# Kernel optimization log

Hardware: AMD Instinct MI355X
Metric: run time of the kernel (lower is better)

The kernel has to match this reference:

```python
import jax, jax.numpy as jnp
import numpy as np

H, QP, VP, D, DP = 4, 4, 4, 128, 64
DH = D // H


def setup_inputs() -> dict:
    key = jax.random.key(0)
    ks = jax.random.split(key, 16)
    B, L = 1, 1024
    w_c0 = float(np.log(np.e - 1.0))
    inp = {
        'single': jax.random.normal(ks[0], (B, L, D), jnp.float32),
        'pair': jax.random.normal(ks[1], (B, L, L, DP), jnp.float32),
        'T': jax.random.normal(ks[2], (B, L, 4, 4), jnp.float32),
        'w_C': jnp.full((H,), w_c0, jnp.float32),
        'ln_g': jnp.ones((D,), jnp.float32),
        'ln_b': jnp.zeros((D,), jnp.float32),
        'Wq': jax.random.normal(ks[3], (D, H * DH), jnp.float32) * 0.05,
        'Wk': jax.random.normal(ks[4], (D, H * DH), jnp.float32) * 0.05,
        'Wv': jax.random.normal(ks[5], (D, H * DH), jnp.float32) * 0.05,
        'Wqpt': jax.random.normal(ks[6], (D, H * QP * 3), jnp.float32) * 0.05,
        'Wkpt': jax.random.normal(ks[7], (D, H * QP * 3), jnp.float32) * 0.05,
        'Wvpt': jax.random.normal(ks[8], (D, H * VP * 3), jnp.float32) * 0.05,
        'Wb': jax.random.normal(ks[9], (DP, H), jnp.float32) * 0.05,
        'Wout': jax.random.normal(ks[10], (H * (DH + DP + VP * 3 + VP), D), jnp.float32) * 0.05,
        'b_out': jnp.zeros((D,), jnp.float32),
    }
    return inp


def _layernorm(x, g, b, eps=1e-5):
    x32 = x.astype(jnp.float32)
    mu = x32.mean(-1, keepdims=True)
    var = ((x32 - mu) ** 2).mean(-1, keepdims=True)
    return ((x32 - mu) * jax.lax.rsqrt(var + eps) * g + b).astype(x.dtype)


def reference(single, pair, T, w_C, ln_g, ln_b, Wq, Wk, Wv, Wqpt, Wkpt, Wvpt, Wb, Wout, b_out):
    B, L, Dm = single.shape
    scale_attn = DH ** (-0.5)
    z = _layernorm(single, ln_g, ln_b)
    Q = (z @ Wq).reshape(B, L, H, DH)
    K = (z @ Wk).reshape(B, L, H, DH)
    V = (z @ Wv).reshape(B, L, H, DH)
    Q_pt = (z @ Wqpt).reshape(B, L, H, QP, 3)
    K_pt = (z @ Wkpt).reshape(B, L, H, QP, 3)
    V_pt = (z @ Wvpt).reshape(B, L, H, VP, 3)
    R = T[..., :3, :3]   # [B,L,3,3]
    t = T[..., :3, 3]    # [B,L,3]
    # global-frame points: R @ p + t
    Q_g = jnp.einsum('blxy,blhpy->blhpx', R, Q_pt) + t[:, :, None, None, :]
    K_g = jnp.einsum('blxy,blhpy->blhpx', R, K_pt) + t[:, :, None, None, :]
    V_g = jnp.einsum('blxy,blhpy->blhpx', R, V_pt) + t[:, :, None, None, :]
    # scalar QK score [B,H,L,L]
    s_attn = jnp.einsum('bihd,bjhd->bhij', Q, K) * scale_attn
    # pair bias [B,H,L,L]
    b_attn = jnp.einsum('bijc,ch->bhij', pair, Wb)
    # squared point distance [B,H,L,L]
    diff = Q_g[:, :, None] - K_g[:, None]          # [B,L,L,H,QP,3]
    d2 = jnp.moveaxis((diff ** 2).sum((-1, -2)), -1, 1)
    w_pt = jax.nn.softplus(w_C)[None, :, None, None]
    attn = jax.nn.softmax(s_attn + b_attn - 0.5 * w_pt * d2, axis=-1)
    # scalar values [B,L,H*DH]
    o_s = jnp.einsum('bhij,bjhd->bihd', attn, V).reshape(B, L, H * DH)
    # point values aggregated in global frame then mapped back: R^T (p - t)
    o_pt_g = jnp.einsum('bhij,bjhpx->bihpx', attn, V_g)
    o_pt = jnp.einsum('blyx,blhpy->blhpx', R, o_pt_g - t[:, :, None, None, :])
    o_pt_n = jnp.sqrt((o_pt ** 2).sum(-1))
    # pair aggregation [B,L,H*DP]
    o_pair = jnp.einsum('bhij,bijc->bihc', attn, pair).reshape(B, L, H * DP)
    out = jnp.concatenate([o_s, o_pair, o_pt.reshape(B, L, -1), o_pt_n.reshape(B, L, -1)], axis=-1)
    return single + out @ Wout + b_out
```

## Files before the change

kernel.cpp:

```cpp
#include <hip/hip_runtime.h>
#include <math.h>

#define L_SEQ 1024
#define DM 128

#define OFF_KHAT 0
#define OFF_QHAT (L_SEQ * 192)
#define OFF_V    (OFF_QHAT + L_SEQ * 192)
#define OFF_VG   (OFF_V + L_SEQ * DM)

typedef __attribute__((address_space(1))) const void* gas_t;
typedef __attribute__((address_space(3))) void* las_t;

__device__ __forceinline__ void async16(const float4* g, float4* l) {
    __builtin_amdgcn_global_load_lds((gas_t)g, (las_t)l, 16, 0, 0);
}

__global__ __launch_bounds__(256) void ipa_prep(
    const float* __restrict__ single, const float* __restrict__ T,
    const float* __restrict__ w_C, const float* __restrict__ ln_g, const float* __restrict__ ln_b,
    const float* __restrict__ Wq, const float* __restrict__ Wk, const float* __restrict__ Wv,
    const float* __restrict__ Wqpt, const float* __restrict__ Wkpt, const float* __restrict__ Wvpt,
    float* __restrict__ ws)
{
    __shared__ float z_lds[128];
    __shared__ float proj[528];
    __shared__ float qg[4][4][3];
    __shared__ float kg[4][4][3];
    __shared__ float cq[4], ck[4];

    const int t = threadIdx.x;
    const int i = blockIdx.x;

    if (t < 64) {
        float x0 = single[i*DM + t];
        float x1 = single[i*DM + 64 + t];
        float s = x0 + x1, s2 = x0*x0 + x1*x1;
        #pragma unroll
        for (int off = 1; off < 64; off <<= 1) { s += __shfl_xor(s, off); s2 += __shfl_xor(s2, off); }
        float mu = s * 0.0078125f;
        float var = s2 * 0.0078125f - mu*mu;
        float rs = rsqrtf(var + 1e-5f);
        z_lds[t]      = (x0 - mu) * rs * ln_g[t]      + ln_b[t];
        z_lds[t + 64] = (x1 - mu) * rs * ln_g[t + 64] + ln_b[t + 64];
    }
    __syncthreads();

    for (int cc = t; cc < 528; cc += 256) {
        const float* W; int col, ncol;
        if (cc < 128)      { W = Wq;   col = cc;       ncol = 128; }
        else if (cc < 256) { W = Wk;   col = cc - 128; ncol = 128; }
        else if (cc < 384) { W = Wv;   col = cc - 256; ncol = 128; }
        else if (cc < 432) { W = Wqpt; col = cc - 384; ncol = 48;  }
        else if (cc < 480) { W = Wkpt; col = cc - 432; ncol = 48;  }
        else               { W = Wvpt; col = cc - 480; ncol = 48;  }
        float a = 0.f;
        #pragma unroll 8
        for (int k = 0; k < 128; ++k)
            a = fmaf(z_lds[k], W[k*ncol + col], a);
        proj[cc] = a;
    }
    __syncthreads();

    if (t < 16) {
        int h = t >> 2, p = t & 3;
        float R[3][3], tt[3];
        #pragma unroll
        for (int x = 0; x < 3; ++x) {
            #pragma unroll
            for (int y = 0; y < 3; ++y) R[x][y] = T[i*16 + x*4 + y];
            tt[x] = T[i*16 + x*4 + 3];
        }
        int base = 384 + (h*4 + p)*3;
        float q0 = proj[base],    q1 = proj[base+1],  q2 = proj[base+2];
        float k0 = proj[base+48], k1 = proj[base+49], k2 = proj[base+50];
        float v0 = proj[base+96], v1 = proj[base+97], v2 = proj[base+98];
        #pragma unroll
        for (int x = 0; x < 3; ++x) {
            float qq = R[x][0]*q0 + R[x][1]*q1 + R[x][2]*q2 + tt[x];
            float kk = R[x][0]*k0 + R[x][1]*k1 + R[x][2]*k2 + tt[x];
            float vv = R[x][0]*v0 + R[x][1]*v1 + R[x][2]*v2 + tt[x];
            qg[h][p][x] = qq;
            kg[h][p][x] = kk;
            ws[OFF_VG + (size_t)i*48 + h*12 + p*3 + x] = vv;
        }
    }
    __syncthreads();

    if (t < 8) {
        int h = t >> 1, isk = t & 1;
        float w = w_C[h];
        float wp = log1pf(__expf(w));
        float sq = 0.f;
        #pragma unroll
        for (int p = 0; p < 4; ++p)
            #pragma unroll
            for (int x = 0; x < 3; ++x) {
                float g = isk ? kg[h][p][x] : qg[h][p][x];
                sq += g*g;
            }
        float c = -0.5f * wp * sq;
        if (isk) ck[h] = c; else cq[h] = c;
    }
    __syncthreads();

    if (t < 128) ws[OFF_V + (size_t)i*DM + t] = proj[256 + t];
    const float scale_attn = 0.17677669529663687f;
    if (t < 192) {
        int h = t / 48, k = t % 48;
        float w = w_C[h];
        float wp = log1pf(__expf(w));
        float kv, qv;
        if (k < 32) {
            kv = proj[128 + h*32 + k];
            qv = scale_attn * proj[h*32 + k];
        } else if (k < 44) {
            int e = k - 32;
            kv = kg[h][e/3][e%3];
            qv = wp * qg[h][e/3][e%3];
        } else if (k == 44) { kv = ck[h]; qv = 1.0f; }
        else if (k == 45)   { kv = 1.0f; qv = cq[h]; }
        else                { kv = 0.f;  qv = 0.f; }
        ws[OFF_KHAT + (size_t)i*192 + t] = kv;
        ws[OFF_QHAT + (size_t)i*192 + t] = qv;
    }
}

__global__ __launch_bounds__(256, 2) void ipa_attn(
    const float* __restrict__ single, const float* __restrict__ pair,
    const float* __restrict__ T, const float* __restrict__ Wb,
    const float* __restrict__ Wout, const float* __restrict__ b_out,
    const float* __restrict__ ws, float* __restrict__ out)
{
    __shared__ __align__(16) float4 pair_w[4][2][2][16][16];
    __shared__ __align__(16) float4 qhat_lds[2][4][13];
    __shared__ __align__(16) float wbt_lds[4][68];
    __shared__ __align__(16) float p_ws[4][2][16][4];

    const int t = threadIdx.x;
    const int wv = t >> 6, lane = t & 63;
    const int i0 = blockIdx.x * 2;

    if (t < 96) {
        int r = t / 48, rest = t % 48;
        qhat_lds[r][rest/12][rest%12] = ((const float4*)(ws + OFF_QHAT))[(size_t)(i0+r)*48 + rest];
    } else if (t < 160) {
        int c = t - 96;
        float4 w4 = ((const float4*)Wb)[c];
        wbt_lds[0][c] = w4.x; wbt_lds[1][c] = w4.y; wbt_lds[2][c] = w4.z; wbt_lds[3][c] = w4.w;
    }

    const int m_h  = lane & 3,  m_j  = lane >> 2;
    const int os_h = lane >> 4, os_jh = (lane >> 3) & 1, os_d4 = lane & 7;
    const int op_c4 = lane & 15, op_jq = lane >> 4;
    const int og_he = lane & 15, og_jq = lane >> 4;
    const bool og_act = og_he < 12;
    const int og_h  = (og_act ? og_he : 0) / 3;
    const int og_ix = og_act ? og_he : 0;

    float m0_run = -INFINITY, l0_run = 0.f;
    float m1_run = -INFINITY, l1_run = 0.f;
    float4 accp[2][4];
    float4 accs[2], accg[2];
    #pragma unroll
    for (int r = 0; r < 2; ++r) {
        accs[r] = make_float4(0.f,0.f,0.f,0.f);
        accg[r] = make_float4(0.f,0.f,0.f,0.f);
        #pragma unroll
        for (int h = 0; h < 4; ++h) accp[r][h] = make_float4(0.f,0.f,0.f,0.f);
    }

    const float4* pair4 = (const float4*)pair;
    const float4* kh4   = (const float4*)(ws + OFF_KHAT);
    const float4* v4    = (const float4*)(ws + OFF_V);
    const float4* vg4   = (const float4*)(ws + OFF_VG);
    float4* mypair = &pair_w[wv][0][0][0][0];

    #pragma unroll
    for (int it = 0; it < 8; ++it) {
        int idx = it*64 + lane;
        int row = idx >> 8, j = (idx >> 4) & 15, slot = idx & 15;
        int c4 = slot ^ (j & 7);
        async16(pair4 + ((size_t)(i0+row)*L_SEQ + wv*256 + j)*16 + c4, mypair + idx);
    }
    __syncthreads();

    for (int s = 0; s < 16; ++s) {
        const int cur = s & 1;
        const int j0 = wv*256 + s*16;

        float4 kh[12];
        {
            const float4* kp = kh4 + (size_t)(j0 + m_j)*48 + m_h*12;
            #pragma unroll
            for (int k4 = 0; k4 < 12; ++k4) kh[k4] = kp[k4];
        }
        float4 vv[8];
        #pragma unroll
        for (int jj = 0; jj < 8; ++jj)
            vv[jj] = v4[(size_t)(j0 + os_jh*8 + jj)*32 + os_h*8 + os_d4];
        float4 gvv[4];
        #pragma unroll
        for (int jj = 0; jj < 4; ++jj)
            gvv[jj] = vg4[(size_t)(j0 + og_jq*4 + jj)*12 + og_ix];

        if (s + 1 < 16) {
            #pragma unroll
            for (int it = 0; it < 8; ++it) {
                int idx = it*64 + lane;
                int row = idx >> 8, j = (idx >> 4) & 15, slot = idx & 15;
                int c4 = slot ^ (j & 7);
                async16(pair4 + ((size_t)(i0+row)*L_SEQ + wv*256 + (s+1)*16 + j)*16 + c4,
                        mypair + (1 - cur)*512 + idx);
            }
            asm volatile("s_waitcnt vmcnt(32)" ::: "memory");
        } else {
            asm volatile("s_waitcnt vmcnt(24)" ::: "memory");
        }

        const float4* prow0 = mypair + cur*512 +       m_j*16;
        const float4* prow1 = mypair + cur*512 + 256 + m_j*16;
        const float4* wrow  = (const float4*)&wbt_lds[m_h][0];
        float b0 = 0.f, b1 = 0.f;
        #pragma unroll
        for (int cc = 0; cc < 16; ++cc) {
            int sw = cc ^ (m_j & 7);
            float4 wh  = wrow[cc];
            float4 pv0 = prow0[sw];
            float4 pv1 = prow1[sw];
            b0 += pv0.x*wh.x + pv0.y*wh.y + pv0.z*wh.z + pv0.w*wh.w;
            b1 += pv1.x*wh.x + pv1.y*wh.y + pv1.z*wh.z + pv1.w*wh.w;
        }
        float d0a=0.f, d0b=0.f, d1a=0.f, d1b=0.f;
        #pragma unroll
        for (int k4 = 0; k4 < 12; k4 += 2) {
            float4 q0a = qhat_lds[0][m_h][k4], q0b = qhat_lds[0][m_h][k4+1];
            float4 q1a = qhat_lds[1][m_h][k4], q1b = qhat_lds[1][m_h][k4+1];
            float4 ka = kh[k4], kb = kh[k4+1];
            d0a = fmaf(ka.x, q0a.x, d0a); d0a = fmaf(ka.y, q0a.y, d0a);
            d0a = fmaf(ka.z, q0a.z, d0a); d0a = fmaf(ka.w, q0a.w, d0a);
            d0b = fmaf(kb.x, q0b.x, d0b); d0b = fmaf(kb.y, q0b.y, d0b);
            d0b = fmaf(kb.z, q0b.z, d0b); d0b = fmaf(kb.w, q0b.w, d0b);
            d1a = fmaf(ka.x, q1a.x, d1a); d1a = fmaf(ka.y, q1a.y, d1a);
            d1a = fmaf(ka.z, q1a.z, d1a); d1a = fmaf(ka.w, q1a.w, d1a);
            d1b = fmaf(kb.x, q1b.x, d1b); d1b = fmaf(kb.y, q1b.y, d1b);
            d1b = fmaf(kb.z, q1b.z, d1b); d1b = fmaf(kb.w, q1b.w, d1b);
        }
        float logit0 = d0a + d0b + b0;
        float logit1 = d1a + d1b + b1;

        float c0 = logit0, c1 = logit1;
        #pragma unroll
        for (int off = 4; off < 64; off <<= 1) {
            c0 = fmaxf(c0, __shfl_xor(c0, off));
            c1 = fmaxf(c1, __shfl_xor(c1, off));
        }
        float mn0 = fmaxf(m0_run, c0), mn1 = fmaxf(m1_run, c1);
        float al0 = __expf(m0_run - mn0), al1 = __expf(m1_run - mn1);
        float p0 = __expf(logit0 - mn0), p1 = __expf(logit1 - mn1);
        l0_run = l0_run * al0 + p0;  l1_run = l1_run * al1 + p1;
        m0_run = mn0;  m1_run = mn1;
        p_ws[wv][0][m_j][m_h] = p0;
        p_ws[wv][1][m_j][m_h] = p1;
        float a00 = __shfl(al0, 0), a01 = __shfl(al0, 1), a02 = __shfl(al0, 2), a03 = __shfl(al0, 3);
        float a10 = __shfl(al1, 0), a11 = __shfl(al1, 1), a12 = __shfl(al1, 2), a13 = __shfl(al1, 3);
        asm volatile("" ::: "memory");

        accp[0][0].x *= a00; accp[0][0].y *= a00; accp[0][0].z *= a00; accp[0][0].w *= a00;
        accp[0][1].x *= a01; accp[0][1].y *= a01; accp[0][1].z *= a01; accp[0][1].w *= a01;
        accp[0][2].x *= a02; accp[0][2].y *= a02; accp[0][2].z *= a02; accp[0][2].w *= a02;
        accp[0][3].x *= a03; accp[0][3].y *= a03; accp[0][3].z *= a03; accp[0][3].w *= a03;
        accp[1][0].x *= a10; accp[1][0].y *= a10; accp[1][0].z *= a10; accp[1][0].w *= a10;
        accp[1][1].x *= a11; accp[1][1].y *= a11; accp[1][1].z *= a11; accp[1][1].w *= a11;
        accp[1][2].x *= a12; accp[1][2].y *= a12; accp[1][2].z *= a12; accp[1][2].w *= a12;
        accp[1][3].x *= a13; accp[1][3].y *= a13; accp[1][3].z *= a13; accp[1][3].w *= a13;
        float as0 = (os_h & 2) ? ((os_h & 1) ? a03 : a02) : ((os_h & 1) ? a01 : a00);
        float as1 = (os_h & 2) ? ((os_h & 1) ? a13 : a12) : ((os_h & 1) ? a11 : a10);
        float ag0 = (og_h & 2) ? ((og_h & 1) ? a03 : a02) : ((og_h & 1) ? a01 : a00);
        float ag1 = (og_h & 2) ? ((og_h & 1) ? a13 : a12) : ((og_h & 1) ? a11 : a10);
        accs[0].x *= as0; accs[0].y *= as0; accs[0].z *= as0; accs[0].w *= as0;
        accs[1].x *= as1; accs[1].y *= as1; accs[1].z *= as1; accs[1].w *= as1;
        accg[0].x *= ag0; accg[0].y *= ag0; accg[0].z *= ag0; accg[0].w *= ag0;
        accg[1].x *= ag1; accg[1].y *= ag1; accg[1].z *= ag1; accg[1].w *= ag1;

        #pragma unroll
        for (int jj = 0; jj < 4; ++jj) {
            int j = op_jq*4 + jj;
            int sw = op_c4 ^ (j & 7);
            float4 pv0 = mypair[cur*512 +       j*16 + sw];
            float4 pv1 = mypair[cur*512 + 256 + j*16 + sw];
            float4 pj0 = *(const float4*)&p_ws[wv][0][j][0];
            float4 pj1 = *(const float4*)&p_ws[wv][1][j][0];
            accp[0][0].x = fmaf(pj0.x, pv0.x, accp[0][0].x); accp[0][0].y = fmaf(pj0.x, pv0.y, accp[0][0].y);
            accp[0][0].z = fmaf(pj0.x, pv0.z, accp[0][0].z); accp[0][0].w = fmaf(pj0.x, pv0.w, accp[0][0].w);
            accp[0][1].x = fmaf(pj0.y, pv0.x, accp[0][1].x); accp[0][1].y = fmaf(pj0.y, pv0.y, accp[0][1].y);
            accp[0][1].z = fmaf(pj0.y, pv0.z, accp[0][1].z); accp[0][1].w = fmaf(pj0.y, pv0.w, accp[0][1].w);
            accp[0][2].x = fmaf(pj0.z, pv0.x, accp[0][2].x); accp[0][2].y = fmaf(pj0.z, pv0.y, accp[0][2].y);
            accp[0][2].z = fmaf(pj0.z, pv0.z, accp[0][2].z); accp[0][2].w = fmaf(pj0.z, pv0.w, accp[0][2].w);
            accp[0][3].x = fmaf(pj0.w, pv0.x, accp[0][3].x); accp[0][3].y = fmaf(pj0.w, pv0.y, accp[0][3].y);
            accp[0][3].z = fmaf(pj0.w, pv0.z, accp[0][3].z); accp[0][3].w = fmaf(pj0.w, pv0.w, accp[0][3].w);
            accp[1][0].x = fmaf(pj1.x, pv1.x, accp[1][0].x); accp[1][0].y = fmaf(pj1.x, pv1.y, accp[1][0].y);
            accp[1][0].z = fmaf(pj1.x, pv1.z, accp[1][0].z); accp[1][0].w = fmaf(pj1.x, pv1.w, accp[1][0].w);
            accp[1][1].x = fmaf(pj1.y, pv1.x, accp[1][1].x); accp[1][1].y = fmaf(pj1.y, pv1.y, accp[1][1].y);
            accp[1][1].z = fmaf(pj1.y, pv1.z, accp[1][1].z); accp[1][1].w = fmaf(pj1.y, pv1.w, accp[1][1].w);
            accp[1][2].x = fmaf(pj1.z, pv1.x, accp[1][2].x); accp[1][2].y = fmaf(pj1.z, pv1.y, accp[1][2].y);
            accp[1][2].z = fmaf(pj1.z, pv1.z, accp[1][2].z); accp[1][2].w = fmaf(pj1.z, pv1.w, accp[1][2].w);
            accp[1][3].x = fmaf(pj1.w, pv1.x, accp[1][3].x); accp[1][3].y = fmaf(pj1.w, pv1.y, accp[1][3].y);
            accp[1][3].z = fmaf(pj1.w, pv1.z, accp[1][3].z); accp[1][3].w = fmaf(pj1.w, pv1.w, accp[1][3].w);
        }
        #pragma unroll
        for (int jj = 0; jj < 8; ++jj) {
            int j = os_jh*8 + jj;
            float pa0 = p_ws[wv][0][j][os_h];
            float pa1 = p_ws[wv][1][j][os_h];
            accs[0].x = fmaf(pa0, vv[jj].x, accs[0].x); accs[0].y = fmaf(pa0, vv[jj].y, accs[0].y);
            accs[0].z = fmaf(pa0, vv[jj].z, accs[0].z); accs[0].w = fmaf(pa0, vv[jj].w, accs[0].w);
            accs[1].x = fmaf(pa1, vv[jj].x, accs[1].x); accs[1].y = fmaf(pa1, vv[jj].y, accs[1].y);
            accs[1].z = fmaf(pa1, vv[jj].z, accs[1].z); accs[1].w = fmaf(pa1, vv[jj].w, accs[1].w);
        }
        #pragma unroll
        for (int jj = 0; jj < 4; ++jj) {
            int j = og_jq*4 + jj;
            float pg0 = og_act ? p_ws[wv][0][j][og_h] : 0.f;
            float pg1 = og_act ? p_ws[wv][1][j][og_h] : 0.f;
            accg[0].x = fmaf(pg0, gvv[jj].x, accg[0].x); accg[0].y = fmaf(pg0, gvv[jj].y, accg[0].y);
            accg[0].z = fmaf(pg0, gvv[jj].z, accg[0].z); accg[0].w = fmaf(pg0, gvv[jj].w, accg[0].w);
            accg[1].x = fmaf(pg1, gvv[jj].x, accg[1].x); accg[1].y = fmaf(pg1, gvv[jj].y, accg[1].y);
            accg[1].z = fmaf(pg1, gvv[jj].z, accg[1].z); accg[1].w = fmaf(pg1, gvv[jj].w, accg[1].w);
        }
    }

    #pragma unroll
    for (int off = 4; off < 64; off <<= 1) { l0_run += __shfl_xor(l0_run, off); l1_run += __shfl_xor(l1_run, off); }
    #pragma unroll
    for (int r = 0; r < 2; ++r) {
        #pragma unroll
        for (int h = 0; h < 4; ++h) {
            #pragma unroll
            for (int off = 16; off < 64; off <<= 1) {
                accp[r][h].x += __shfl_xor(accp[r][h].x, off);
                accp[r][h].y += __shfl_xor(accp[r][h].y, off);
                accp[r][h].z += __shfl_xor(accp[r][h].z, off);
                accp[r][h].w += __shfl_xor(accp[r][h].w, off);
            }
        }
        accs[r].x += __shfl_xor(accs[r].x, 8); accs[r].y += __shfl_xor(accs[r].y, 8);
        accs[r].z += __shfl_xor(accs[r].z, 8); accs[r].w += __shfl_xor(accs[r].w, 8);
        #pragma unroll
        for (int off = 16; off < 64; off <<= 1) {
            accg[r].x += __shfl_xor(accg[r].x, off); accg[r].y += __shfl_xor(accg[r].y, off);
            accg[r].z += __shfl_xor(accg[r].z, off); accg[r].w += __shfl_xor(accg[r].w, off);
        }
    }

    float* scratch = (float*)&pair_w[0][0][0][0][0];
    float* cw = scratch + wv*4096;
    #pragma unroll
    for (int r = 0; r < 2; ++r) {
        if (lane < 16) {
            #pragma unroll
            for (int h = 0; h < 4; ++h)
                *(float4*)&cw[r*512 + h*64 + op_c4*4] = accp[r][h];
        }
        if (os_jh == 0) *(float4*)&cw[r*512 + 256 + os_h*32 + os_d4*4] = accs[r];
        if (lane < 12)  *(float4*)&cw[r*512 + 384 + lane*4] = accg[r];
        if (lane < 4) {
            cw[r*512 + 432 + m_h] = (r == 0) ? l0_run : l1_run;
            cw[r*512 + 436 + m_h] = (r == 0) ? m0_run : m1_run;
        }
    }
    __syncthreads();

    const int EP = 1024;
    float* u   = scratch + EP;
    float* og2 = scratch + EP + 896;
    float* wts = scratch + EP + 992;
    float* ivs = scratch + EP + 1024;

    if (t < 8) {
        int r = t >> 2, h = t & 3;
        float m0 = scratch[0*4096 + r*512 + 436 + h], m1 = scratch[1*4096 + r*512 + 436 + h];
        float m2 = scratch[2*4096 + r*512 + 436 + h], m3 = scratch[3*4096 + r*512 + 436 + h];
        float M = fmaxf(fmaxf(m0, m1), fmaxf(m2, m3));
        float w0 = __expf(m0 - M), w1 = __expf(m1 - M);
        float w2 = __expf(m2 - M), w3 = __expf(m3 - M);
        float L = scratch[0*4096 + r*512 + 432 + h]*w0 + scratch[1*4096 + r*512 + 432 + h]*w1
                + scratch[2*4096 + r*512 + 432 + h]*w2 + scratch[3*4096 + r*512 + 432 + h]*w3;
        wts[r*16 + 0 + h] = w0; wts[r*16 + 4 + h] = w1;
        wts[r*16 + 8 + h] = w2; wts[r*16 + 12 + h] = w3;
        ivs[r*4 + h] = 1.f / L;
    }
    __syncthreads();

    {
        int r = t >> 7, q = t & 127;
        const float* wt = wts + r*16;
        const float* iv = ivs + r*4;
        {
            int hs = q >> 5;
            float v = scratch[0*4096 + r*512 + 256 + q]*wt[0 + hs] + scratch[1*4096 + r*512 + 256 + q]*wt[4 + hs]
                    + scratch[2*4096 + r*512 + 256 + q]*wt[8 + hs] + scratch[3*4096 + r*512 + 256 + q]*wt[12 + hs];
            u[r*448 + q] = v * iv[hs];
        }
        #pragma unroll
        for (int pp = 0; pp < 2; ++pp) {
            int idx = pp*128 + q;
            int hp = idx >> 6;
            float v = scratch[0*4096 + r*512 + idx]*wt[0 + hp] + scratch[1*4096 + r*512 + idx]*wt[4 + hp]
                    + scratch[2*4096 + r*512 + idx]*wt[8 + hp] + scratch[3*4096 + r*512 + idx]*wt[12 + hp];
            u[r*448 + 128 + idx] = v * iv[hp];
        }
        if (t < 96) {
            int r2 = t / 48, qg = t % 48, hg = qg / 12;
            const float* wt2 = wts + r2*16;
            float v = scratch[0*4096 + r2*512 + 384 + qg]*wt2[0 + hg] + scratch[1*4096 + r2*512 + 384 + qg]*wt2[4 + hg]
                    + scratch[2*4096 + r2*512 + 384 + qg]*wt2[8 + hg] + scratch[3*4096 + r2*512 + 384 + qg]*wt2[12 + hg];
            og2[r2*48 + qg] = v * ivs[r2*4 + hg];
        }
    }
    __syncthreads();

    if (t < 32) {
        int r = t >> 4, idx = t & 15, h = idx >> 2, p = idx & 3;
        int ii = i0 + r;
        float R[3][3], tt[3];
        #pragma unroll
        for (int x = 0; x < 3; ++x) {
            #pragma unroll
            for (int y = 0; y < 3; ++y) R[x][y] = T[ii*16 + x*4 + y];
            tt[x] = T[ii*16 + x*4 + 3];
        }
        float v0 = og2[r*48 + h*12 + p*3+0] - tt[0];
        float v1 = og2[r*48 + h*12 + p*3+1] - tt[1];
        float v2 = og2[r*48 + h*12 + p*3+2] - tt[2];
        float n2 = 0.f;
        #pragma unroll
        for (int x = 0; x < 3; ++x) {
            float o = R[0][x]*v0 + R[1][x]*v1 + R[2][x]*v2;
            u[r*448 + 384 + h*12 + p*3 + x] = o;
            n2 += o*o;
        }
        u[r*448 + 432 + h*4 + p] = sqrtf(n2);
    }
    __syncthreads();

    {
        int r = t >> 7, d = t & 127;
        int ii = i0 + r;
        float acc = single[ii*DM + d] + b_out[d];
        const float4* u4 = (const float4*)(u + r*448);
        #pragma unroll 4
        for (int k4 = 0; k4 < 112; ++k4) {
            float4 uu = u4[k4];
            const float* wp = Wout + (size_t)(k4*4)*128 + d;
            acc = fmaf(uu.x, wp[0],   acc);
            acc = fmaf(uu.y, wp[128], acc);
            acc = fmaf(uu.z, wp[256], acc);
            acc = fmaf(uu.w, wp[384], acc);
        }
        out[ii*DM + d] = acc;
    }
}

extern "C" void kernel_launch(void* const* d_in, const int* in_sizes, int n_in,
                              void* d_out, int out_size, void* d_ws, size_t ws_size,
                              hipStream_t stream)
{
    const float* single = (const float*)d_in[0];
    const float* pair   = (const float*)d_in[1];
    const float* T      = (const float*)d_in[2];
    const float* w_C    = (const float*)d_in[3];
    const float* ln_g   = (const float*)d_in[4];
    const float* ln_b   = (const float*)d_in[5];
    const float* Wq     = (const float*)d_in[6];
    const float* Wk     = (const float*)d_in[7];
    const float* Wv     = (const float*)d_in[8];
    const float* Wqpt   = (const float*)d_in[9];
    const float* Wkpt   = (const float*)d_in[10];
    const float* Wvpt   = (const float*)d_in[11];
    const float* Wb     = (const float*)d_in[12];
    const float* Wout   = (const float*)d_in[13];
    const float* b_out  = (const float*)d_in[14];
    float* out = (float*)d_out;
    float* ws  = (float*)d_ws;

    ipa_prep<<<1024, 256, 0, stream>>>(single, T, w_C, ln_g, ln_b, Wq, Wk, Wv, Wqpt, Wkpt, Wvpt, ws);
    ipa_attn<<<512, 256, 0, stream>>>(single, pair, T, Wb, Wout, b_out, ws, out);
}
```

Baseline: 519.9 us.

## Split attention blocks into two 4-wave groups with per-head waves over 32-key chunks

```diff
diff --git a/kernel.cpp b/kernel.cpp
--- a/kernel.cpp
+++ b/kernel.cpp
@@ -3,6 +3,8 @@
 
 #define L_SEQ 1024
 #define DM 128
+#define JC 32
+#define NCH 16
 
 #define OFF_KHAT 0
 #define OFF_QHAT (L_SEQ * 192)
@@ -15,6 +17,8 @@
 __device__ __forceinline__ void async16(const float4* g, float4* l) {
     __builtin_amdgcn_global_load_lds((gas_t)g, (las_t)l, 16, 0, 0);
 }
+#define ASYNC_BAR() asm volatile("s_waitcnt lgkmcnt(0)\n\ts_barrier" ::: "memory")
+#define VM_DRAIN()  asm volatile("s_waitcnt vmcnt(0)" ::: "memory")
 
 __global__ __launch_bounds__(256) void ipa_prep(
     const float* __restrict__ single, const float* __restrict__ T,
@@ -126,42 +130,58 @@
     }
 }
 
-__global__ __launch_bounds__(256, 2) void ipa_attn(
+__global__ __launch_bounds__(512, 4) void ipa_attn(
     const float* __restrict__ single, const float* __restrict__ pair,
     const float* __restrict__ T, const float* __restrict__ Wb,
     const float* __restrict__ Wout, const float* __restrict__ b_out,
     const float* __restrict__ ws, float* __restrict__ out)
 {
-    __shared__ __align__(16) float4 pair_w[4][2][2][16][16];
+    __shared__ __align__(16) float4 pair_w[2][2][2][32][16];
     __shared__ __align__(16) float4 qhat_lds[2][4][13];
-    __shared__ __align__(16) float wbt_lds[4][68];
-    __shared__ __align__(16) float p_ws[4][2][16][4];
+    __shared__ __align__(16) float  wbt_lds[4][68];
+    __shared__ __align__(16) float  p_lds[2][4][2][32];
+    __shared__ float alpha_lds[2][4][2];
 
     const int t = threadIdx.x;
-    const int wv = t >> 6, lane = t & 63;
+    const int w = t >> 6, lane = t & 63;
+    const int g = w >> 2, hw = w & 3;
+    const int gt = t & 255;
     const int i0 = blockIdx.x * 2;
 
+    const int j_s = lane & 31, kc = lane >> 5;
+    const int d4  = lane & 7,  jg_s = lane >> 3;
+    const int c4p = lane >> 4, jg_p = lane & 15;
+    const int g4  = lane & 3,  jg_g = lane >> 2;
+    const int g4c = (g4 < 3) ? g4 : 0;
+
+    float4* pwf = &pair_w[0][0][0][0][0];
+    float4* gp  = pwf + g*2048;
+    const float4* pair4 = (const float4*)pair;
+    const float4* kh4   = (const float4*)(ws + OFF_KHAT);
+    const float4* qh4   = (const float4*)(ws + OFF_QHAT);
+    const float4* v4    = (const float4*)(ws + OFF_V);
+    const float4* vg4   = (const float4*)(ws + OFF_VG);
+    const float4* wbt4  = (const float4*)&wbt_lds[0][0];
+
+    #pragma unroll
+    for (int it = 0; it < 4; ++it) {
+        int idx = it*256 + gt;
+        int row = idx >> 9, j = (idx >> 4) & 31, slot = idx & 15;
+        int c4 = slot ^ (j & 7);
+        async16(pair4 + ((size_t)(i0+row)*L_SEQ + g*512 + j)*16 + c4, gp + idx);
+    }
     if (t < 96) {
         int r = t / 48, rest = t % 48;
-        qhat_lds[r][rest/12][rest%12] = ((const float4*)(ws + OFF_QHAT))[(size_t)(i0+r)*48 + rest];
+        qhat_lds[r][rest/12][rest%12] = qh4[(size_t)(i0+r)*48 + rest];
     } else if (t < 160) {
         int c = t - 96;
         float4 w4 = ((const float4*)Wb)[c];
         wbt_lds[0][c] = w4.x; wbt_lds[1][c] = w4.y; wbt_lds[2][c] = w4.z; wbt_lds[3][c] = w4.w;
     }
-
-    const int m_h  = lane & 3,  m_j  = lane >> 2;
-    const int os_h = lane >> 4, os_jh = (lane >> 3) & 1, os_d4 = lane & 7;
-    const int op_c4 = lane & 15, op_jq = lane >> 4;
-    const int og_he = lane & 15, og_jq = lane >> 4;
-    const bool og_act = og_he < 12;
-    const int og_h  = (og_act ? og_he : 0) / 3;
-    const int og_ix = og_act ? og_he : 0;
-
-    float m0_run = -INFINITY, l0_run = 0.f;
-    float m1_run = -INFINITY, l1_run = 0.f;
-    float4 accp[2][4];
-    float4 accs[2], accg[2];
+    __syncthreads();
+
+    float m0r = -INFINITY, m1r = -INFINITY, l0r = 0.f, l1r = 0.f;
+    float4 accp[2][4], accs[2], accg[2];
     #pragma unroll
     for (int r = 0; r < 2; ++r) {
         accs[r] = make_float4(0.f,0.f,0.f,0.f);
@@ -170,62 +190,29 @@
         for (int h = 0; h < 4; ++h) accp[r][h] = make_float4(0.f,0.f,0.f,0.f);
     }
 
-    const float4* pair4 = (const float4*)pair;
-    const float4* kh4   = (const float4*)(ws + OFF_KHAT);
-    const float4* v4    = (const float4*)(ws + OFF_V);
-    const float4* vg4   = (const float4*)(ws + OFF_VG);
-    float4* mypair = &pair_w[wv][0][0][0][0];
-
-    #pragma unroll
-    for (int it = 0; it < 8; ++it) {
-        int idx = it*64 + lane;
-        int row = idx >> 8, j = (idx >> 4) & 15, slot = idx & 15;
-        int c4 = slot ^ (j & 7);
-        async16(pair4 + ((size_t)(i0+row)*L_SEQ + wv*256 + j)*16 + c4, mypair + idx);
-    }
-    __syncthreads();
-
-    for (int s = 0; s < 16; ++s) {
-        const int cur = s & 1;
-        const int j0 = wv*256 + s*16;
-
-        float4 kh[12];
+    for (int ch = 0; ch < NCH; ++ch) {
+        const int cur = ch & 1;
+        const int j0 = g*512 + ch*JC;
+
+        VM_DRAIN();
+        ASYNC_BAR();
+
+        float4 kh[6];
         {
-            const float4* kp = kh4 + (size_t)(j0 + m_j)*48 + m_h*12;
-            #pragma unroll
-            for (int k4 = 0; k4 < 12; ++k4) kh[k4] = kp[k4];
-        }
-        float4 vv[8];
-        #pragma unroll
-        for (int jj = 0; jj < 8; ++jj)
-            vv[jj] = v4[(size_t)(j0 + os_jh*8 + jj)*32 + os_h*8 + os_d4];
-        float4 gvv[4];
-        #pragma unroll
-        for (int jj = 0; jj < 4; ++jj)
-            gvv[jj] = vg4[(size_t)(j0 + og_jq*4 + jj)*12 + og_ix];
-
-        if (s + 1 < 16) {
-            #pragma unroll
-            for (int it = 0; it < 8; ++it) {
-                int idx = it*64 + lane;
-                int row = idx >> 8, j = (idx >> 4) & 15, slot = idx & 15;
-                int c4 = slot ^ (j & 7);
-                async16(pair4 + ((size_t)(i0+row)*L_SEQ + wv*256 + (s+1)*16 + j)*16 + c4,
-                        mypair + (1 - cur)*512 + idx);
-            }
-            asm volatile("s_waitcnt vmcnt(32)" ::: "memory");
-        } else {
-            asm volatile("s_waitcnt vmcnt(24)" ::: "memory");
-        }
-
-        const float4* prow0 = mypair + cur*512 +       m_j*16;
-        const float4* prow1 = mypair + cur*512 + 256 + m_j*16;
-        const float4* wrow  = (const float4*)&wbt_lds[m_h][0];
+            const float4* kp = kh4 + (size_t)(j0 + j_s)*48 + hw*12 + kc*6;
+            #pragma unroll
+            for (int k4 = 0; k4 < 6; ++k4) kh[k4] = kp[k4];
+        }
+
+        const float4* prow0 = gp + cur*1024 +       j_s*16;
+        const float4* prow1 = gp + cur*1024 + 512 + j_s*16;
+        const float4* wrow  = wbt4 + hw*17;
         float b0 = 0.f, b1 = 0.f;
         #pragma unroll
-        for (int cc = 0; cc < 16; ++cc) {
-            int sw = cc ^ (m_j & 7);
-            float4 wh  = wrow[cc];
+        for (int cq = 0; cq < 8; ++cq) {
+            int c4 = kc*8 + cq;
+            int sw = c4 ^ (j_s & 7);
+            float4 wh  = wrow[c4];
             float4 pv0 = prow0[sw];
             float4 pv1 = prow1[sw];
             b0 += pv0.x*wh.x + pv0.y*wh.y + pv0.z*wh.z + pv0.w*wh.w;
@@ -233,9 +220,9 @@
         }
         float d0a=0.f, d0b=0.f, d1a=0.f, d1b=0.f;
         #pragma unroll
-        for (int k4 = 0; k4 < 12; k4 += 2) {
-            float4 q0a = qhat_lds[0][m_h][k4], q0b = qhat_lds[0][m_h][k4+1];
-            float4 q1a = qhat_lds[1][m_h][k4], q1b = qhat_lds[1][m_h][k4+1];
+        for (int k4 = 0; k4 < 6; k4 += 2) {
+            float4 q0a = qhat_lds[0][hw][kc*6+k4], q0b = qhat_lds[0][hw][kc*6+k4+1];
+            float4 q1a = qhat_lds[1][hw][kc*6+k4], q1b = qhat_lds[1][hw][kc*6+k4+1];
             float4 ka = kh[k4], kb = kh[k4+1];
             d0a = fmaf(ka.x, q0a.x, d0a); d0a = fmaf(ka.y, q0a.y, d0a);
             d0a = fmaf(ka.z, q0a.z, d0a); d0a = fmaf(ka.w, q0a.w, d0a);
@@ -246,177 +233,184 @@
             d1b = fmaf(kb.x, q1b.x, d1b); d1b = fmaf(kb.y, q1b.y, d1b);
             d1b = fmaf(kb.z, q1b.z, d1b); d1b = fmaf(kb.w, q1b.w, d1b);
         }
-        float logit0 = d0a + d0b + b0;
-        float logit1 = d1a + d1b + b1;
+        float part0 = d0a + d0b + b0;
+        float part1 = d1a + d1b + b1;
+        float logit0 = part0 + __shfl_xor(part0, 32);
+        float logit1 = part1 + __shfl_xor(part1, 32);
 
         float c0 = logit0, c1 = logit1;
         #pragma unroll
-        for (int off = 4; off < 64; off <<= 1) {
+        for (int off = 1; off < 32; off <<= 1) {
             c0 = fmaxf(c0, __shfl_xor(c0, off));
             c1 = fmaxf(c1, __shfl_xor(c1, off));
         }
-        float mn0 = fmaxf(m0_run, c0), mn1 = fmaxf(m1_run, c1);
-        float al0 = __expf(m0_run - mn0), al1 = __expf(m1_run - mn1);
+        float mn0 = fmaxf(m0r, c0), mn1 = fmaxf(m1r, c1);
+        float al0 = __expf(m0r - mn0), al1 = __expf(m1r - mn1);
         float p0 = __expf(logit0 - mn0), p1 = __expf(logit1 - mn1);
-        l0_run = l0_run * al0 + p0;  l1_run = l1_run * al1 + p1;
-        m0_run = mn0;  m1_run = mn1;
-        p_ws[wv][0][m_j][m_h] = p0;
-        p_ws[wv][1][m_j][m_h] = p1;
-        float a00 = __shfl(al0, 0), a01 = __shfl(al0, 1), a02 = __shfl(al0, 2), a03 = __shfl(al0, 3);
-        float a10 = __shfl(al1, 0), a11 = __shfl(al1, 1), a12 = __shfl(al1, 2), a13 = __shfl(al1, 3);
-        asm volatile("" ::: "memory");
-
-        accp[0][0].x *= a00; accp[0][0].y *= a00; accp[0][0].z *= a00; accp[0][0].w *= a00;
-        accp[0][1].x *= a01; accp[0][1].y *= a01; accp[0][1].z *= a01; accp[0][1].w *= a01;
-        accp[0][2].x *= a02; accp[0][2].y *= a02; accp[0][2].z *= a02; accp[0][2].w *= a02;
-        accp[0][3].x *= a03; accp[0][3].y *= a03; accp[0][3].z *= a03; accp[0][3].w *= a03;
-        accp[1][0].x *= a10; accp[1][0].y *= a10; accp[1][0].z *= a10; accp[1][0].w *= a10;
-        accp[1][1].x *= a11; accp[1][1].y *= a11; accp[1][1].z *= a11; accp[1][1].w *= a11;
-        accp[1][2].x *= a12; accp[1][2].y *= a12; accp[1][2].z *= a12; accp[1][2].w *= a12;
-        accp[1][3].x *= a13; accp[1][3].y *= a13; accp[1][3].z *= a13; accp[1][3].w *= a13;
-        float as0 = (os_h & 2) ? ((os_h & 1) ? a03 : a02) : ((os_h & 1) ? a01 : a00);
-        float as1 = (os_h & 2) ? ((os_h & 1) ? a13 : a12) : ((os_h & 1) ? a11 : a10);
-        float ag0 = (og_h & 2) ? ((og_h & 1) ? a03 : a02) : ((og_h & 1) ? a01 : a00);
-        float ag1 = (og_h & 2) ? ((og_h & 1) ? a13 : a12) : ((og_h & 1) ? a11 : a10);
-        accs[0].x *= as0; accs[0].y *= as0; accs[0].z *= as0; accs[0].w *= as0;
-        accs[1].x *= as1; accs[1].y *= as1; accs[1].z *= as1; accs[1].w *= as1;
-        accg[0].x *= ag0; accg[0].y *= ag0; accg[0].z *= ag0; accg[0].w *= ag0;
-        accg[1].x *= ag1; accg[1].y *= ag1; accg[1].z *= ag1; accg[1].w *= ag1;
-
-        #pragma unroll
-        for (int jj = 0; jj < 4; ++jj) {
-            int j = op_jq*4 + jj;
-            int sw = op_c4 ^ (j & 7);
-            float4 pv0 = mypair[cur*512 +       j*16 + sw];
-            float4 pv1 = mypair[cur*512 + 256 + j*16 + sw];
-            float4 pj0 = *(const float4*)&p_ws[wv][0][j][0];
-            float4 pj1 = *(const float4*)&p_ws[wv][1][j][0];
-            accp[0][0].x = fmaf(pj0.x, pv0.x, accp[0][0].x); accp[0][0].y = fmaf(pj0.x, pv0.y, accp[0][0].y);
-            accp[0][0].z = fmaf(pj0.x, pv0.z, accp[0][0].z); accp[0][0].w = fmaf(pj0.x, pv0.w, accp[0][0].w);
-            accp[0][1].x = fmaf(pj0.y, pv0.x, accp[0][1].x); accp[0][1].y = fmaf(pj0.y, pv0.y, accp[0][1].y);
-            accp[0][1].z = fmaf(pj0.y, pv0.z, accp[0][1].z); accp[0][1].w = fmaf(pj0.y, pv0.w, accp[0][1].w);
-            accp[0][2].x = fmaf(pj0.z, pv0.x, accp[0][2].x); accp[0][2].y = fmaf(pj0.z, pv0.y, accp[0][2].y);
-            accp[0][2].z = fmaf(pj0.z, pv0.z, accp[0][2].z); accp[0][2].w = fmaf(pj0.z, pv0.w, accp[0][2].w);
-            accp[0][3].x = fmaf(pj0.w, pv0.x, accp[0][3].x); accp[0][3].y = fmaf(pj0.w, pv0.y, accp[0][3].y);
-            accp[0][3].z = fmaf(pj0.w, pv0.z, accp[0][3].z); accp[0][3].w = fmaf(pj0.w, pv0.w, accp[0][3].w);
-            accp[1][0].x = fmaf(pj1.x, pv1.x, accp[1][0].x); accp[1][0].y = fmaf(pj1.x, pv1.y, accp[1][0].y);
-            accp[1][0].z = fmaf(pj1.x, pv1.z, accp[1][0].z); accp[1][0].w = fmaf(pj1.x, pv1.w, accp[1][0].w);
-            accp[1][1].x = fmaf(pj1.y, pv1.x, accp[1][1].x); accp[1][1].y = fmaf(pj1.y, pv1.y, accp[1][1].y);
-            accp[1][1].z = fmaf(pj1.y, pv1.z, accp[1][1].z); accp[1][1].w = fmaf(pj1.y, pv1.w, accp[1][1].w);
-            accp[1][2].x = fmaf(pj1.z, pv1.x, accp[1][2].x); accp[1][2].y = fmaf(pj1.z, pv1.y, accp[1][2].y);
-            accp[1][2].z = fmaf(pj1.z, pv1.z, accp[1][2].z); accp[1][2].w = fmaf(pj1.z, pv1.w, accp[1][2].w);
-            accp[1][3].x = fmaf(pj1.w, pv1.x, accp[1][3].x); accp[1][3].y = fmaf(pj1.w, pv1.y, accp[1][3].y);
-            accp[1][3].z = fmaf(pj1.w, pv1.z, accp[1][3].z); accp[1][3].w = fmaf(pj1.w, pv1.w, accp[1][3].w);
-        }
-        #pragma unroll
-        for (int jj = 0; jj < 8; ++jj) {
-            int j = os_jh*8 + jj;
-            float pa0 = p_ws[wv][0][j][os_h];
-            float pa1 = p_ws[wv][1][j][os_h];
-            accs[0].x = fmaf(pa0, vv[jj].x, accs[0].x); accs[0].y = fmaf(pa0, vv[jj].y, accs[0].y);
-            accs[0].z = fmaf(pa0, vv[jj].z, accs[0].z); accs[0].w = fmaf(pa0, vv[jj].w, accs[0].w);
-            accs[1].x = fmaf(pa1, vv[jj].x, accs[1].x); accs[1].y = fmaf(pa1, vv[jj].y, accs[1].y);
-            accs[1].z = fmaf(pa1, vv[jj].z, accs[1].z); accs[1].w = fmaf(pa1, vv[jj].w, accs[1].w);
-        }
-        #pragma unroll
-        for (int jj = 0; jj < 4; ++jj) {
-            int j = og_jq*4 + jj;
-            float pg0 = og_act ? p_ws[wv][0][j][og_h] : 0.f;
-            float pg1 = og_act ? p_ws[wv][1][j][og_h] : 0.f;
-            accg[0].x = fmaf(pg0, gvv[jj].x, accg[0].x); accg[0].y = fmaf(pg0, gvv[jj].y, accg[0].y);
-            accg[0].z = fmaf(pg0, gvv[jj].z, accg[0].z); accg[0].w = fmaf(pg0, gvv[jj].w, accg[0].w);
-            accg[1].x = fmaf(pg1, gvv[jj].x, accg[1].x); accg[1].y = fmaf(pg1, gvv[jj].y, accg[1].y);
-            accg[1].z = fmaf(pg1, gvv[jj].z, accg[1].z); accg[1].w = fmaf(pg1, gvv[jj].w, accg[1].w);
+        l0r = l0r*al0 + p0;  l1r = l1r*al1 + p1;
+        m0r = mn0;  m1r = mn1;
+        if (kc == 0) { p_lds[g][hw][0][j_s] = p0; p_lds[g][hw][1][j_s] = p1; }
+        if (lane == 0) { alpha_lds[g][hw][0] = al0; alpha_lds[g][hw][1] = al1; }
+
+        float4 vv[4];
+        #pragma unroll
+        for (int jj = 0; jj < 4; ++jj)
+            vv[jj] = v4[(size_t)(j0 + jg_s + 8*jj)*32 + hw*8 + d4];
+        float4 gvv[2];
+        #pragma unroll
+        for (int jj = 0; jj < 2; ++jj)
+            gvv[jj] = vg4[(size_t)(j0 + jg_g + 16*jj)*12 + hw*3 + g4c];
+
+        if (ch + 1 < NCH) {
+            #pragma unroll
+            for (int it = 0; it < 4; ++it) {
+                int idx = it*256 + gt;
+                int row = idx >> 9, j = (idx >> 4) & 31, slot = idx & 15;
+                int c4 = slot ^ (j & 7);
+                async16(pair4 + ((size_t)(i0+row)*L_SEQ + g*512 + (ch+1)*JC + j)*16 + c4,
+                        gp + (1-cur)*1024 + idx);
+            }
+        }
+        ASYNC_BAR();
+
+        {
+            float al[4][2];
+            #pragma unroll
+            for (int h = 0; h < 4; ++h) { al[h][0] = alpha_lds[g][h][0]; al[h][1] = alpha_lds[g][h][1]; }
+            #pragma unroll
+            for (int r = 0; r < 2; ++r)
+                #pragma unroll
+                for (int h = 0; h < 4; ++h) {
+                    float a = al[h][r];
+                    accp[r][h].x *= a; accp[r][h].y *= a; accp[r][h].z *= a; accp[r][h].w *= a;
+                }
+            accs[0].x *= al0; accs[0].y *= al0; accs[0].z *= al0; accs[0].w *= al0;
+            accs[1].x *= al1; accs[1].y *= al1; accs[1].z *= al1; accs[1].w *= al1;
+            accg[0].x *= al0; accg[0].y *= al0; accg[0].z *= al0; accg[0].w *= al0;
+            accg[1].x *= al1; accg[1].y *= al1; accg[1].z *= al1; accg[1].w *= al1;
+
+            #pragma unroll
+            for (int jj = 0; jj < 2; ++jj) {
+                int j = jg_p + 16*jj;
+                int sw = (hw*4 + c4p) ^ (j & 7);
+                float4 pv0 = gp[cur*1024 +       j*16 + sw];
+                float4 pv1 = gp[cur*1024 + 512 + j*16 + sw];
+                float p00 = p_lds[g][0][0][j], p01 = p_lds[g][1][0][j];
+                float p02 = p_lds[g][2][0][j], p03 = p_lds[g][3][0][j];
+                float p10 = p_lds[g][0][1][j], p11 = p_lds[g][1][1][j];
+                float p12 = p_lds[g][2][1][j], p13 = p_lds[g][3][1][j];
+                accp[0][0].x = fmaf(p00, pv0.x, accp[0][0].x); accp[0][0].y = fmaf(p00, pv0.y, accp[0][0].y);
+                accp[0][0].z = fmaf(p00, pv0.z, accp[0][0].z); accp[0][0].w = fmaf(p00, pv0.w, accp[0][0].w);
+                accp[0][1].x = fmaf(p01, pv0.x, accp[0][1].x); accp[0][1].y = fmaf(p01, pv0.y, accp[0][1].y);
+                accp[0][1].z = fmaf(p01, pv0.z, accp[0][1].z); accp[0][1].w = fmaf(p01, pv0.w, accp[0][1].w);
+                accp[0][2].x = fmaf(p02, pv0.x, accp[0][2].x); accp[0][2].y = fmaf(p02, pv0.y, accp[0][2].y);
+                accp[0][2].z = fmaf(p02, pv0.z, accp[0][2].z); accp[0][2].w = fmaf(p02, pv0.w, accp[0][2].w);
+                accp[0][3].x = fmaf(p03, pv0.x, accp[0][3].x); accp[0][3].y = fmaf(p03, pv0.y, accp[0][3].y);
+                accp[0][3].z = fmaf(p03, pv0.z, accp[0][3].z); accp[0][3].w = fmaf(p03, pv0.w, accp[0][3].w);
+                accp[1][0].x = fmaf(p10, pv1.x, accp[1][0].x); accp[1][0].y = fmaf(p10, pv1.y, accp[1][0].y);
+                accp[1][0].z = fmaf(p10, pv1.z, accp[1][0].z); accp[1][0].w = fmaf(p10, pv1.w, accp[1][0].w);
+                accp[1][1].x = fmaf(p11, pv1.x, accp[1][1].x); accp[1][1].y = fmaf(p11, pv1.y, accp[1][1].y);
+                accp[1][1].z = fmaf(p11, pv1.z, accp[1][1].z); accp[1][1].w = fmaf(p11, pv1.w, accp[1][1].w);
+                accp[1][2].x = fmaf(p12, pv1.x, accp[1][2].x); accp[1][2].y = fmaf(p12, pv1.y, accp[1][2].y);
+                accp[1][2].z = fmaf(p12, pv1.z, accp[1][2].z); accp[1][2].w = fmaf(p12, pv1.w, accp[1][2].w);
+                accp[1][3].x = fmaf(p13, pv1.x, accp[1][3].x); accp[1][3].y = fmaf(p13, pv1.y, accp[1][3].y);
+                accp[1][3].z = fmaf(p13, pv1.z, accp[1][3].z); accp[1][3].w = fmaf(p13, pv1.w, accp[1][3].w);
+            }
+            #pragma unroll
+            for (int jj = 0; jj < 4; ++jj) {
+                int j = jg_s + 8*jj;
+                float pa0 = p_lds[g][hw][0][j], pa1 = p_lds[g][hw][1][j];
+                accs[0].x = fmaf(pa0, vv[jj].x, accs[0].x); accs[0].y = fmaf(pa0, vv[jj].y, accs[0].y);
+                accs[0].z = fmaf(pa0, vv[jj].z, accs[0].z); accs[0].w = fmaf(pa0, vv[jj].w, accs[0].w);
+                accs[1].x = fmaf(pa1, vv[jj].x, accs[1].x); accs[1].y = fmaf(pa1, vv[jj].y, accs[1].y);
+                accs[1].z = fmaf(pa1, vv[jj].z, accs[1].z); accs[1].w = fmaf(pa1, vv[jj].w, accs[1].w);
+            }
+            #pragma unroll
+            for (int jj = 0; jj < 2; ++jj) {
+                int j = jg_g + 16*jj;
+                float pg0 = p_lds[g][hw][0][j], pg1 = p_lds[g][hw][1][j];
+                accg[0].x = fmaf(pg0, gvv[jj].x, accg[0].x); accg[0].y = fmaf(pg0, gvv[jj].y, accg[0].y);
+                accg[0].z = fmaf(pg0, gvv[jj].z, accg[0].z); accg[0].w = fmaf(pg0, gvv[jj].w, accg[0].w);
+                accg[1].x = fmaf(pg1, gvv[jj].x, accg[1].x); accg[1].y = fmaf(pg1, gvv[jj].y, accg[1].y);
+                accg[1].z = fmaf(pg1, gvv[jj].z, accg[1].z); accg[1].w = fmaf(pg1, gvv[jj].w, accg[1].w);
+            }
         }
     }
 
     #pragma unroll
-    for (int off = 4; off < 64; off <<= 1) { l0_run += __shfl_xor(l0_run, off); l1_run += __shfl_xor(l1_run, off); }
+    for (int off = 1; off < 32; off <<= 1) { l0r += __shfl_xor(l0r, off); l1r += __shfl_xor(l1r, off); }
     #pragma unroll
     for (int r = 0; r < 2; ++r) {
         #pragma unroll
-        for (int h = 0; h < 4; ++h) {
-            #pragma unroll
-            for (int off = 16; off < 64; off <<= 1) {
+        for (int h = 0; h < 4; ++h)
+            #pragma unroll
+            for (int off = 1; off < 16; off <<= 1) {
                 accp[r][h].x += __shfl_xor(accp[r][h].x, off);
                 accp[r][h].y += __shfl_xor(accp[r][h].y, off);
                 accp[r][h].z += __shfl_xor(accp[r][h].z, off);
                 accp[r][h].w += __shfl_xor(accp[r][h].w, off);
             }
-        }
-        accs[r].x += __shfl_xor(accs[r].x, 8); accs[r].y += __shfl_xor(accs[r].y, 8);
-        accs[r].z += __shfl_xor(accs[r].z, 8); accs[r].w += __shfl_xor(accs[r].w, 8);
-        #pragma unroll
-        for (int off = 16; off < 64; off <<= 1) {
+        #pragma unroll
+        for (int off = 8; off < 64; off <<= 1) {
+            accs[r].x += __shfl_xor(accs[r].x, off); accs[r].y += __shfl_xor(accs[r].y, off);
+            accs[r].z += __shfl_xor(accs[r].z, off); accs[r].w += __shfl_xor(accs[r].w, off);
+        }
+        #pragma unroll
+        for (int off = 4; off < 64; off <<= 1) {
             accg[r].x += __shfl_xor(accg[r].x, off); accg[r].y += __shfl_xor(accg[r].y, off);
             accg[r].z += __shfl_xor(accg[r].z, off); accg[r].w += __shfl_xor(accg[r].w, off);
         }
     }
 
-    float* scratch = (float*)&pair_w[0][0][0][0][0];
-    float* cw = scratch + wv*4096;
+    float* scratch = (float*)pwf;
+    float* cw = scratch + g*8192;
     #pragma unroll
     for (int r = 0; r < 2; ++r) {
-        if (lane < 16) {
+        if ((lane & 15) == 0) {
             #pragma unroll
             for (int h = 0; h < 4; ++h)
-                *(float4*)&cw[r*512 + h*64 + op_c4*4] = accp[r][h];
-        }
-        if (os_jh == 0) *(float4*)&cw[r*512 + 256 + os_h*32 + os_d4*4] = accs[r];
-        if (lane < 12)  *(float4*)&cw[r*512 + 384 + lane*4] = accg[r];
-        if (lane < 4) {
-            cw[r*512 + 432 + m_h] = (r == 0) ? l0_run : l1_run;
-            cw[r*512 + 436 + m_h] = (r == 0) ? m0_run : m1_run;
-        }
-    }
-    __syncthreads();
-
-    const int EP = 1024;
-    float* u   = scratch + EP;
-    float* og2 = scratch + EP + 896;
-    float* wts = scratch + EP + 992;
-    float* ivs = scratch + EP + 1024;
+                *(float4*)&cw[r*512 + h*64 + (hw*4 + (lane>>4))*4] = accp[r][h];
+        }
+        if (lane < 8) *(float4*)&cw[r*512 + 256 + hw*32 + lane*4] = accs[r];
+        if (lane < 3) *(float4*)&cw[r*512 + 384 + hw*12 + lane*4] = accg[r];
+    }
+    if (lane == 0) {
+        cw[0*512 + 432 + hw] = l0r; cw[0*512 + 436 + hw] = m0r;
+        cw[1*512 + 432 + hw] = l1r; cw[1*512 + 436 + hw] = m1r;
+    }
+    __syncthreads();
+
+    float* u   = scratch + 2048;
+    float* og2 = scratch + 2048 + 896;
+    float* wts = scratch + 2048 + 992;
+    float* ivs = scratch + 2048 + 1008;
+    float* tmp = scratch + 2048 + 1024;
 
     if (t < 8) {
         int r = t >> 2, h = t & 3;
-        float m0 = scratch[0*4096 + r*512 + 436 + h], m1 = scratch[1*4096 + r*512 + 436 + h];
-        float m2 = scratch[2*4096 + r*512 + 436 + h], m3 = scratch[3*4096 + r*512 + 436 + h];
-        float M = fmaxf(fmaxf(m0, m1), fmaxf(m2, m3));
-        float w0 = __expf(m0 - M), w1 = __expf(m1 - M);
-        float w2 = __expf(m2 - M), w3 = __expf(m3 - M);
-        float L = scratch[0*4096 + r*512 + 432 + h]*w0 + scratch[1*4096 + r*512 + 432 + h]*w1
-                + scratch[2*4096 + r*512 + 432 + h]*w2 + scratch[3*4096 + r*512 + 432 + h]*w3;
-        wts[r*16 + 0 + h] = w0; wts[r*16 + 4 + h] = w1;
-        wts[r*16 + 8 + h] = w2; wts[r*16 + 12 + h] = w3;
+        float mA = scratch[r*512 + 436 + h], mB = scratch[8192 + r*512 + 436 + h];
+        float M = fmaxf(mA, mB);
+        float wA = __expf(mA - M), wB = __expf(mB - M);
+        float L = scratch[r*512 + 432 + h]*wA + scratch[8192 + r*512 + 432 + h]*wB;
+        wts[r*8 + h] = wA; wts[r*8 + 4 + h] = wB;
         ivs[r*4 + h] = 1.f / L;
     }
     __syncthreads();
 
     {
-        int r = t >> 7, q = t & 127;
-        const float* wt = wts + r*16;
-        const float* iv = ivs + r*4;
-        {
-            int hs = q >> 5;
-            float v = scratch[0*4096 + r*512 + 256 + q]*wt[0 + hs] + scratch[1*4096 + r*512 + 256 + q]*wt[4 + hs]
-                    + scratch[2*4096 + r*512 + 256 + q]*wt[8 + hs] + scratch[3*4096 + r*512 + 256 + q]*wt[12 + hs];
-            u[r*448 + q] = v * iv[hs];
-        }
-        #pragma unroll
-        for (int pp = 0; pp < 2; ++pp) {
-            int idx = pp*128 + q;
-            int hp = idx >> 6;
-            float v = scratch[0*4096 + r*512 + idx]*wt[0 + hp] + scratch[1*4096 + r*512 + idx]*wt[4 + hp]
-                    + scratch[2*4096 + r*512 + idx]*wt[8 + hp] + scratch[3*4096 + r*512 + idx]*wt[12 + hp];
-            u[r*448 + 128 + idx] = v * iv[hp];
-        }
-        if (t < 96) {
-            int r2 = t / 48, qg = t % 48, hg = qg / 12;
-            const float* wt2 = wts + r2*16;
-            float v = scratch[0*4096 + r2*512 + 384 + qg]*wt2[0 + hg] + scratch[1*4096 + r2*512 + 384 + qg]*wt2[4 + hg]
-                    + scratch[2*4096 + r2*512 + 384 + qg]*wt2[8 + hg] + scratch[3*4096 + r2*512 + 384 + qg]*wt2[12 + hg];
-            og2[r2*48 + qg] = v * ivs[r2*4 + hg];
-        }
+        int r = t >> 8, q = t & 255, hp = q >> 6;
+        float v = scratch[r*512 + q]*wts[r*8 + hp] + scratch[8192 + r*512 + q]*wts[r*8 + 4 + hp];
+        u[r*448 + 128 + q] = v * ivs[r*4 + hp];
+    }
+    if (t < 256) {
+        int r = t >> 7, q = t & 127, hs = q >> 5;
+        float v = scratch[r*512 + 256 + q]*wts[r*8 + hs] + scratch[8192 + r*512 + 256 + q]*wts[r*8 + 4 + hs];
+        u[r*448 + q] = v * ivs[r*4 + hs];
+    }
+    if (t < 96) {
+        int r = t / 48, qg = t % 48, hg = qg / 12;
+        float v = scratch[r*512 + 384 + qg]*wts[r*8 + hg] + scratch[8192 + r*512 + 384 + qg]*wts[r*8 + 4 + hg];
+        og2[r*48 + qg] = v * ivs[r*4 + hg];
     }
     __syncthreads();
 
@@ -445,12 +439,12 @@
     __syncthreads();
 
     {
-        int r = t >> 7, d = t & 127;
+        int r = (t >> 7) & 1, d = t & 127, kq = t >> 8;
         int ii = i0 + r;
-        float acc = single[ii*DM + d] + b_out[d];
+        float acc = 0.f;
         const float4* u4 = (const float4*)(u + r*448);
         #pragma unroll 4
-        for (int k4 = 0; k4 < 112; ++k4) {
+        for (int k4 = kq*56; k4 < kq*56 + 56; ++k4) {
             float4 uu = u4[k4];
             const float* wp = Wout + (size_t)(k4*4)*128 + d;
             acc = fmaf(uu.x, wp[0],   acc);
@@ -458,7 +452,9 @@
             acc = fmaf(uu.z, wp[256], acc);
             acc = fmaf(uu.w, wp[384], acc);
         }
-        out[ii*DM + d] = acc;
+        if (kq) tmp[r*128 + d] = acc;
+        __syncthreads();
+        if (!kq) out[(size_t)ii*DM + d] = single[(size_t)ii*DM + d] + b_out[d] + acc + tmp[r*128 + d];
     }
 }
 
@@ -485,5 +481,5 @@
     float* ws  = (float*)d_ws;
 
     ipa_prep<<<1024, 256, 0, stream>>>(single, T, w_C, ln_g, ln_b, Wq, Wk, Wv, Wqpt, Wkpt, Wvpt, ws);
-    ipa_attn<<<512, 256, 0, stream>>>(single, pair, T, Wb, Wout, b_out, ws, out);
+    ipa_attn<<<512, 512, 0, stream>>>(single, pair, T, Wb, Wout, b_out, ws, out);
 }
```

New measurement: 617.6 us. +18.8%, slower.
